# Optimization experiments

Hardware: AMD Instinct MI355X
Metric: run time of the kernel (lower is better)

## Reference

```python
import jax, jax.numpy as jnp
import numpy as np

B, T, C, H = 4, 2048, 1024, 16
D = C // H


def setup_inputs() -> dict:
    key = jax.random.key(0)
    ks = jax.random.split(key, 5)
    s = C ** -0.5  # keep linear outputs O(1) like standard init
    x = jax.random.normal(ks[0], (B, T, C), dtype=jnp.float32)
    Wq = jax.random.normal(ks[1], (C, C), dtype=jnp.float32) * s
    Wk = jax.random.normal(ks[2], (C, C), dtype=jnp.float32) * s
    Wv = jax.random.normal(ks[3], (C, C), dtype=jnp.float32) * s
    Wproj = jax.random.normal(ks[4], (C, C), dtype=jnp.float32) * s
    alpha_raw = jnp.zeros((1, H, 1, 1), dtype=jnp.float32)
    beta_raw = jnp.zeros((1, H, 1, 1), dtype=jnp.float32)
    state = jnp.zeros((B, H, D, D), dtype=jnp.float32)
    return dict(x=x, Wq=Wq, Wk=Wk, Wv=Wv, Wproj=Wproj,
                alpha_raw=alpha_raw, beta_raw=beta_raw, state=state)


def reference(x, Wq, Wk, Wv, Wproj, alpha_raw, beta_raw, state):
    Bx, Tx, Cx = x.shape
    Hn = alpha_raw.shape[1]
    Dh = Cx // Hn
    # projections (torch Linear: x @ W^T), split heads -> (B, H, T, D)
    def proj(W):
        return (x @ W.T).reshape(Bx, Tx, Hn, Dh).transpose(0, 2, 1, 3)
    q, k, v = proj(Wq), proj(Wk), proj(Wv)
    # F.normalize(k, dim=-1) with eps=1e-12
    k = k / jnp.maximum(jnp.linalg.norm(k, axis=-1, keepdims=True), 1e-12)
    alpha = jax.nn.sigmoid(alpha_raw) * 0.5  # (1, H, 1, 1)
    beta = jax.nn.sigmoid(beta_raw) * 0.5

    def step(st, qkv):
        qt, kt, vt = qkv  # each (B, H, D)
        # y_t = q_t @ state^T
        y = jnp.einsum('bhe,bhde->bhd', qt, st)
        # Mk = state @ k_t
        Mk = jnp.einsum('bhde,bhe->bhd', st, kt)
        st = st - alpha * jnp.einsum('bhd,bhe->bhde', Mk, kt) \
                + beta * jnp.einsum('bhd,bhe->bhde', vt, kt)
        return st, y

    # scan over time: (T, B, H, D)
    qT = q.transpose(2, 0, 1, 3)
    kT = k.transpose(2, 0, 1, 3)
    vT = v.transpose(2, 0, 1, 3)
    state_f, ys = jax.lax.scan(step, state, (qT, kT, vT))
    y = ys.transpose(1, 0, 2, 3).reshape(Bx, Tx, Cx)  # (B, T, C)
    out = y @ Wproj.T
    return out, state_f
```

## Files before the change

kernel.cpp:

```cpp
#include <hip/hip_runtime.h>
#include <hip/hip_bf16.h>
#include <cstdint>

#define B_ 4
#define T_ 2048
#define C_ 1024
#define H_ 16
#define D_ 64
#define NC_ 32
#define L_ 64

typedef __attribute__((ext_vector_type(8))) short bf16x8;
typedef __attribute__((ext_vector_type(4))) float f32x4;

static __device__ __forceinline__ unsigned short f2bf(float f) {
  unsigned u = __float_as_uint(f);
  u += 0x7fff + ((u >> 16) & 1);
  return (unsigned short)(u >> 16);
}
static __device__ __forceinline__ float bf2f(unsigned short b) {
  return __uint_as_float(((unsigned)b) << 16);
}
static __device__ __forceinline__ int swz128(int row, int byte) {
  return row * 128 + (byte ^ ((row & 7) << 4));
}

#define LDS_BARRIER() asm volatile("s_waitcnt lgkmcnt(0)\ns_barrier" ::: "memory")

__global__ __launch_bounds__(256) void cvt_kernel(const float* __restrict__ src,
                                                  unsigned short* __restrict__ dst, int n) {
  int i = (blockIdx.x * 256 + threadIdx.x) * 4;
  if (i >= n) return;
  float4 v = *reinterpret_cast<const float4*>(src + i);
  ushort4 o;
  o.x = f2bf(v.x); o.y = f2bf(v.y); o.z = f2bf(v.z); o.w = f2bf(v.w);
  *reinterpret_cast<ushort4*>(dst + i) = o;
}

__global__ __launch_bounds__(256) void cvt_w_kernel(const float* __restrict__ wq,
                                                    const float* __restrict__ wk,
                                                    const float* __restrict__ wv,
                                                    const float* __restrict__ wp,
                                                    unsigned short* __restrict__ W3,
                                                    unsigned short* __restrict__ Wp) {
  const int g = blockIdx.x >> 10;
  const float* src = (g == 0) ? wq : (g == 1) ? wk : (g == 2) ? wv : wp;
  unsigned short* dst = (g < 3) ? (W3 + (long)g * 1048576) : Wp;
  int i = ((blockIdx.x & 1023) * 256 + threadIdx.x) * 4;
  float4 v = *reinterpret_cast<const float4*>(src + i);
  ushort4 o;
  o.x = f2bf(v.x); o.y = f2bf(v.y); o.z = f2bf(v.z); o.w = f2bf(v.w);
  *reinterpret_cast<ushort4*>(dst + i) = o;
}


#define STAGE256(GP, GR0, KT, LOFF) do {                                          \
    const unsigned short* _s = (GP) + ((GR0) + wid * 8 + lr8) * 1024L             \
                               + (long)(KT) * 64 + skb * 8;                       \
    char* _d = (char*)lds + (LOFF) + wid * 1024;                                  \
    __builtin_amdgcn_global_load_lds((const __attribute__((address_space(1))) void*)_s,      \
        (__attribute__((address_space(3))) void*)_d, 16, 0, 0);                   \
    __builtin_amdgcn_global_load_lds((const __attribute__((address_space(1))) void*)(_s + 64 * 1024L), \
        (__attribute__((address_space(3))) void*)(_d + 8192), 16, 0, 0);          \
  } while (0)

#define PHASE256(AO, BO, MH, NH, STG) do {                                        \
    asm volatile("s_waitcnt vmcnt(6)" ::: "memory");                              \
    bf16x8 av[4][2], bv[2][2];                                                    \
    {                                                                             \
      const char* ab = (const char*)lds + (AO) + (MH) * 16384 + arow;             \
      const char* bb = (const char*)lds + (BO) + (NH) * 16384 + brow;             \
      _Pragma("unroll")                                                           \
      for (int j = 0; j < 4; ++j) {                                               \
        av[j][0] = *(const bf16x8*)(ab + j * 4096 + cb0);                         \
        av[j][1] = *(const bf16x8*)(ab + j * 4096 + cb1);                         \
      }                                                                           \
      _Pragma("unroll")                                                           \
      for (int j2 = 0; j2 < 2; ++j2) {                                            \
        bv[j2][0] = *(const bf16x8*)(bb + j2 * 8192 + cb0);                       \
        bv[j2][1] = *(const bf16x8*)(bb + j2 * 8192 + cb1);                       \
      }                                                                           \
    }                                                                             \
    STG;                                                                          \
    __builtin_amdgcn_s_barrier();                                                 \
    asm volatile("s_waitcnt lgkmcnt(0)" ::: "memory");                            \
    __builtin_amdgcn_sched_barrier(0);                                            \
    __builtin_amdgcn_s_setprio(1);                                                \
    _Pragma("unroll")                                                             \
    for (int j = 0; j < 4; ++j)                                                   \
      _Pragma("unroll")                                                           \
      for (int j2 = 0; j2 < 2; ++j2)                                              \
        acc[(MH) * 4 + j][(NH) * 2 + j2] = __builtin_amdgcn_mfma_f32_16x16x32_bf16( \
            av[j][0], bv[j2][0], acc[(MH) * 4 + j][(NH) * 2 + j2], 0, 0, 0);      \
    _Pragma("unroll")                                                             \
    for (int j = 0; j < 4; ++j)                                                   \
      _Pragma("unroll")                                                           \
      for (int j2 = 0; j2 < 2; ++j2)                                              \
        acc[(MH) * 4 + j][(NH) * 2 + j2] = __builtin_amdgcn_mfma_f32_16x16x32_bf16( \
            av[j][1], bv[j2][1], acc[(MH) * 4 + j][(NH) * 2 + j2], 0, 0, 0);      \
    __builtin_amdgcn_s_setprio(0);                                                \
    __builtin_amdgcn_s_barrier();                                                 \
  } while (0)

__global__ __launch_bounds__(512, 2) void gemm256_bt(
    const unsigned short* __restrict__ A,
    const unsigned short* __restrict__ Bw,
    unsigned short* __restrict__ C, int N) {
  __shared__ __align__(16) char lds[131072];
  enum { EA = 0, EB = 32768, OA = 65536, OB = 98304, HF = 16384 };
  const int tid = threadIdx.x;
  const int wid = tid >> 6, lane = tid & 63;
  const int wm = wid >> 2, wn = wid & 3;
  const int f = lane & 15, g = lane >> 4;
  const int lr8 = lane >> 3, lc = lane & 7;
  const int skb = lc ^ lr8;
  const long bM = (long)blockIdx.y * 256;
  const long bN = (long)blockIdx.x * 256;
  const int cb0 = ((0 + g) ^ (f & 7)) * 16;
  const int cb1 = ((4 + g) ^ (f & 7)) * 16;
  const int arow = (wm * 16 + f) * 128;
  const int brow = (wn * 16 + f) * 128;

  f32x4 acc[8][4] = {};

  STAGE256(A, bM, 0, EA);
  STAGE256(Bw, bN, 0, EB);
  STAGE256(A, bM + 128, 0, EA + HF);
  STAGE256(Bw, bN + 128, 0, EB + HF);
  STAGE256(Bw, bN, 1, OB);
  STAGE256(A, bM, 1, OA);
  asm volatile("s_waitcnt vmcnt(8)" ::: "memory");
  __builtin_amdgcn_s_barrier();

  for (int i = 0; i < 8; ++i) {
    const int todd = 2 * i + 1;
    int te = 2 * i + 2; if (te > 14) te = 14;
    int to = 2 * i + 3; if (to > 15) to = 15;
    PHASE256(EA, EB, 0, 0, STAGE256(A, bM + 128, todd, OA + HF));
    PHASE256(EA, EB, 1, 0, STAGE256(Bw, bN + 128, todd, OB + HF));
    PHASE256(EA, EB, 0, 1, STAGE256(Bw, bN, te, EB));
    PHASE256(EA, EB, 1, 1, STAGE256(A, bM, te, EA));
    PHASE256(OA, OB, 0, 0, STAGE256(A, bM + 128, te, EA + HF));
    PHASE256(OA, OB, 1, 0, STAGE256(Bw, bN + 128, te, EB + HF));
    PHASE256(OA, OB, 0, 1, STAGE256(Bw, bN, to, OB));
    PHASE256(OA, OB, 1, 1, STAGE256(A, bM, to, OA));
  }

#pragma unroll
  for (int mf = 0; mf < 8; ++mf) {
    long row = bM + (mf >> 2) * 128 + (mf & 3) * 32 + wm * 16 + g * 4;
#pragma unroll
    for (int nf = 0; nf < 4; ++nf) {
      long col = bN + (nf >> 1) * 128 + (nf & 1) * 64 + wn * 16 + f;
#pragma unroll
      for (int r = 0; r < 4; ++r)
        C[(row + r) * (long)N + col] = f2bf(acc[mf][nf][r]);
    }
  }
}

template<int OUT_BF16>
__global__ __launch_bounds__(256) void gemm_bt(const unsigned short* __restrict__ A,
                                               const unsigned short* __restrict__ Bw,
                                               void* __restrict__ Cp,
                                               int M, int N, int K) {
  __shared__ __align__(16) unsigned short sA[128 * 32];
  __shared__ __align__(16) unsigned short sB[128 * 32];
  const int tid = threadIdx.x;
  const int wid = tid >> 6, lane = tid & 63;
  const int wm = wid >> 1, wn = wid & 1;
  const long blockM = (long)blockIdx.y * 128;
  const long blockN = (long)blockIdx.x * 128;

  f32x4 acc[4][4] = {};

  const int ar = lane >> 2;
  const int ac = (lane & 3) * 8;
  const unsigned short* Abase = A + (blockM + wid * 32 + ar) * (long)K + ac;
  const unsigned short* Bbase = Bw + (blockN + wid * 32 + ar) * (long)K + ac;
  char* sAb = (char*)sA + wid * 2048;
  char* sBb = (char*)sB + wid * 2048;

  for (int k0 = 0; k0 < K; k0 += 32) {
    __syncthreads();
    __builtin_amdgcn_global_load_lds((const __attribute__((address_space(1))) void*)(Abase + k0),
                                     (__attribute__((address_space(3))) void*)(sAb), 16, 0, 0);
    __builtin_amdgcn_global_load_lds((const __attribute__((address_space(1))) void*)(Abase + 16 * (long)K + k0),
                                     (__attribute__((address_space(3))) void*)(sAb + 1024), 16, 0, 0);
    __builtin_amdgcn_global_load_lds((const __attribute__((address_space(1))) void*)(Bbase + k0),
                                     (__attribute__((address_space(3))) void*)(sBb), 16, 0, 0);
    __builtin_amdgcn_global_load_lds((const __attribute__((address_space(1))) void*)(Bbase + 16 * (long)K + k0),
                                     (__attribute__((address_space(3))) void*)(sBb + 1024), 16, 0, 0);
    __syncthreads();

    const int koff = (lane >> 4) * 8;
    const int rA = wm * 64 + (lane & 15);
    const int rB = wn * 64 + (lane & 15);
    bf16x8 af[4], bfr[4];
#pragma unroll
    for (int m = 0; m < 4; ++m)
      af[m] = *reinterpret_cast<const bf16x8*>(&sA[(rA + m * 16) * 32 + koff]);
#pragma unroll
    for (int n = 0; n < 4; ++n)
      bfr[n] = *reinterpret_cast<const bf16x8*>(&sB[(rB + n * 16) * 32 + koff]);
#pragma unroll
    for (int m = 0; m < 4; ++m)
#pragma unroll
      for (int n = 0; n < 4; ++n)
        acc[m][n] = __builtin_amdgcn_mfma_f32_16x16x32_bf16(af[m], bfr[n], acc[m][n], 0, 0, 0);
  }

  const int cr = (lane >> 4) * 4;
  const int cc = lane & 15;
#pragma unroll
  for (int m = 0; m < 4; ++m) {
    long R = blockM + wm * 64 + m * 16 + cr;
#pragma unroll
    for (int n = 0; n < 4; ++n) {
      long Cc = blockN + wn * 64 + n * 16 + cc;
#pragma unroll
      for (int r = 0; r < 4; ++r) {
        if (OUT_BF16)
          ((unsigned short*)Cp)[(R + r) * (long)N + Cc] = f2bf(acc[m][n][r]);
        else
          ((float*)Cp)[(R + r) * (long)N + Cc] = acc[m][n][r];
      }
    }
  }
}

__global__ __launch_bounds__(256) void chunk_prep(
    unsigned short* __restrict__ qkv,
    const float* __restrict__ a_raw, const float* __restrict__ b_raw,
    unsigned short* __restrict__ Ubuf, unsigned short* __restrict__ Wbuf,
    unsigned short* __restrict__ SLbuf) {
  __shared__ __align__(16) unsigned short sK[64 * 64];
  __shared__ __align__(16) unsigned short sQ[64 * 64];
  __shared__ __align__(16) unsigned short sV[64 * 64];
  __shared__ float sA[64 * 64];

  const int blk = blockIdx.x;
  const int bh = blk >> 5, c = blk & 31;
  const int b = bh >> 4, h = bh & 15;
  const int tid = threadIdx.x;
  const int wid = tid >> 6, lane = tid & 63;

  const float alpha = 0.5f / (1.f + __expf(-a_raw[h]));
  const float beta  = 0.5f / (1.f + __expf(-b_raw[h]));

  {
    const int row = tid >> 2, cg = tid & 3;
    unsigned short* gp = qkv + (long)(b * 2048 + c * 64 + row) * 3072 + h * 64 + cg * 16;
    bf16x8 q0 = *(const bf16x8*)(gp);
    bf16x8 q1 = *(const bf16x8*)(gp + 8);
    bf16x8 k0 = *(const bf16x8*)(gp + 1024);
    bf16x8 k1 = *(const bf16x8*)(gp + 1024 + 8);
    bf16x8 v0 = *(const bf16x8*)(gp + 2048);
    bf16x8 v1 = *(const bf16x8*)(gp + 2048 + 8);
    float kf[16];
    float ss = 0.f;
#pragma unroll
    for (int i = 0; i < 8; ++i) { kf[i] = bf2f((unsigned short)k0[i]); ss += kf[i] * kf[i]; }
#pragma unroll
    for (int i = 0; i < 8; ++i) { kf[8 + i] = bf2f((unsigned short)k1[i]); ss += kf[8 + i] * kf[8 + i]; }
    ss += __shfl_xor(ss, 1);
    ss += __shfl_xor(ss, 2);
    const float inv = 1.f / fmaxf(sqrtf(ss), 1e-12f);
    bf16x8 n0, n1;
#pragma unroll
    for (int i = 0; i < 8; ++i) { n0[i] = (short)f2bf(kf[i] * inv); n1[i] = (short)f2bf(kf[8 + i] * inv); }
    *(bf16x8*)((char*)sK + swz128(row, cg * 32)) = n0;
    *(bf16x8*)((char*)sK + swz128(row, cg * 32 + 16)) = n1;
    *(bf16x8*)(gp + 1024) = n0;
    *(bf16x8*)(gp + 1024 + 8) = n1;
    *(bf16x8*)((char*)sQ + swz128(row, cg * 32)) = q0;
    *(bf16x8*)((char*)sQ + swz128(row, cg * 32 + 16)) = q1;
    *(bf16x8*)((char*)sV + row * 128 + cg * 32) = v0;
    *(bf16x8*)((char*)sV + row * 128 + cg * 32 + 16) = v1;
  }
  __syncthreads();

  const int rfrag = lane & 15, koff = (lane >> 4) * 8, crow = (lane >> 4) * 4;
  const int w2 = wid & 1;
  if (wid < 2) {
#pragma unroll
    for (int mt = 0; mt < 2; ++mt) {
      const int m = w2 * 2 + mt;
      const int ra = 16 * m + rfrag;
      f32x4 acc[4] = {};
#pragma unroll
      for (int ks = 0; ks < 2; ++ks) {
        bf16x8 af = *(const bf16x8*)((const char*)sK + swz128(ra, ks * 64 + koff * 2));
#pragma unroll
        for (int n = 0; n < 4; ++n) {
          bf16x8 bf = *(const bf16x8*)((const char*)sK + swz128(16 * n + rfrag, ks * 64 + koff * 2));
          acc[n] = __builtin_amdgcn_mfma_f32_16x16x32_bf16(af, bf, acc[n], 0, 0, 0);
        }
      }
#pragma unroll
      for (int n = 0; n < 4; ++n)
#pragma unroll
        for (int r = 0; r < 4; ++r)
          sA[(16 * m + crow + r) * 64 + 16 * n + rfrag] = acc[n][r];
    }
  } else {
#pragma unroll
    for (int mt = 0; mt < 2; ++mt) {
      const int m = w2 * 2 + mt;
      const int ra = 16 * m + rfrag;
      f32x4 acc[4] = {};
#pragma unroll
      for (int ks = 0; ks < 2; ++ks) {
        bf16x8 af = *(const bf16x8*)((const char*)sQ + swz128(ra, ks * 64 + koff * 2));
#pragma unroll
        for (int n = 0; n < 4; ++n) {
          bf16x8 bf = *(const bf16x8*)((const char*)sK + swz128(16 * n + rfrag, ks * 64 + koff * 2));
          acc[n] = __builtin_amdgcn_mfma_f32_16x16x32_bf16(af, bf, acc[n], 0, 0, 0);
        }
      }
#pragma unroll
      for (int n = 0; n < 4; ++n)
#pragma unroll
        for (int r = 0; r < 4; ++r) {
          int t = 16 * m + crow + r, j = 16 * n + rfrag;
          SLbuf[(long)blk * 4096 + t * 64 + j] = (j < t) ? f2bf(acc[n][r]) : (unsigned short)0;
        }
    }
  }
  __syncthreads();

  if (wid < 2) {
    const int d = lane;
    float x[64];
#pragma unroll
    for (int t = 0; t < 64; ++t) {
      float rhs;
      if (wid == 0) rhs = beta * bf2f(sV[t * 64 + d]);
      else          rhs = alpha * bf2f(*(const unsigned short*)((const char*)sK + swz128(t, 2 * d)));
      float s = 0.f;
#pragma unroll
      for (int j = 0; j < t; ++j) s = fmaf(sA[t * 64 + j], x[j], s);
      x[t] = rhs - alpha * s;
    }
    unsigned short* ob = (wid == 0 ? Ubuf : Wbuf) + (long)blk * 4096 + d;
#pragma unroll
    for (int t = 0; t < 64; ++t) ob[t * 64] = f2bf(x[t]);
  }
}

__global__ __launch_bounds__(256) void chunk_scan(
    const unsigned short* __restrict__ qkv,
    const unsigned short* __restrict__ Ubuf, const unsigned short* __restrict__ Wbuf,
    const unsigned short* __restrict__ SLbuf,
    const float* __restrict__ state_in, unsigned short* __restrict__ ybuf,
    float* __restrict__ state_out) {
  __shared__ __align__(16) unsigned short sQ[64 * 64];
  __shared__ __align__(16) unsigned short sW[64 * 64];
  __shared__ __align__(16) unsigned short sSL[64 * 64];
  __shared__ __align__(16) unsigned short sKT[64 * 64];
  __shared__ __align__(16) unsigned short sU[64 * 16];
  __shared__ __align__(16) unsigned short sGT[16 * 64];
  __shared__ __align__(16) unsigned short sS[16 * 64];

  const int blk = blockIdx.x;
  const int bh = blk >> 2, dq = blk & 3;
  const int b = bh >> 4, h = bh & 15;
  const int tid = threadIdx.x, wid = tid >> 6, lane = tid & 63;
  const int rfrag = lane & 15, koff = (lane >> 4) * 8, crow = (lane >> 4) * 4;
  const int row = tid >> 2, cg = tid & 3;

  const unsigned short* gpb = qkv + (long)(b * 2048 + row) * 3072 + h * 64 + cg * 16;
  const long tbb = ((long)(bh * 32) * 64 + row) * 64 + cg * 16;
  const long ubb = ((long)(bh * 32) * 64 + (tid >> 1)) * 64 + dq * 16 + (tid & 1) * 8;

  bf16x8 qv0, qv1, kv0, kv1, wv0, wv1, sl0, sl1, uv;
  {
    qv0 = *(const bf16x8*)gpb;
    qv1 = *(const bf16x8*)(gpb + 8);
    kv0 = *(const bf16x8*)(gpb + 1024);
    kv1 = *(const bf16x8*)(gpb + 1024 + 8);
    wv0 = *(const bf16x8*)(Wbuf + tbb);
    wv1 = *(const bf16x8*)(Wbuf + tbb + 8);
    sl0 = *(const bf16x8*)(SLbuf + tbb);
    sl1 = *(const bf16x8*)(SLbuf + tbb + 8);
    uv = (tid < 128) ? *(const bf16x8*)(Ubuf + ubb) : bf16x8{};
  }

  f32x4 sacc;
#pragma unroll
  for (int r = 0; r < 4; ++r)
    sacc[r] = state_in[(long)bh * 4096 + (dq * 16 + crow + r) * 64 + 16 * wid + rfrag];
#pragma unroll
  for (int r = 0; r < 4; ++r)
    *(unsigned short*)((char*)sS + swz128(crow + r, 2 * (16 * wid + rfrag))) = f2bf(sacc[r]);

  for (int c = 0; c < NC_; ++c) {
    *(bf16x8*)((char*)sQ + swz128(row, cg * 32)) = qv0;
    *(bf16x8*)((char*)sQ + swz128(row, cg * 32 + 16)) = qv1;
    *(bf16x8*)((char*)sW + swz128(row, cg * 32)) = wv0;
    *(bf16x8*)((char*)sW + swz128(row, cg * 32 + 16)) = wv1;
    *(bf16x8*)((char*)sSL + swz128(row, cg * 32)) = sl0;
    *(bf16x8*)((char*)sSL + swz128(row, cg * 32 + 16)) = sl1;
#pragma unroll
    for (int i = 0; i < 8; ++i) {
      *(unsigned short*)((char*)sKT + swz128(cg * 16 + i, 2 * row)) = (unsigned short)kv0[i];
      *(unsigned short*)((char*)sKT + swz128(cg * 16 + 8 + i, 2 * row)) = (unsigned short)kv1[i];
    }
    if (tid < 128) *(bf16x8*)((char*)sU + ((tid >> 1) * 16 + (tid & 1) * 8) * 2) = uv;

    {
      const int cn = (c + 1 < NC_) ? c + 1 : c;
      const unsigned short* gp = gpb + (long)cn * 64 * 3072;
      const long tb = tbb + (long)cn * 4096;
      qv0 = *(const bf16x8*)gp;
      qv1 = *(const bf16x8*)(gp + 8);
      kv0 = *(const bf16x8*)(gp + 1024);
      kv1 = *(const bf16x8*)(gp + 1024 + 8);
      wv0 = *(const bf16x8*)(Wbuf + tb);
      wv1 = *(const bf16x8*)(Wbuf + tb + 8);
      sl0 = *(const bf16x8*)(SLbuf + tb);
      sl1 = *(const bf16x8*)(SLbuf + tb + 8);
      if (tid < 128) uv = *(const bf16x8*)(Ubuf + ubb + (long)cn * 4096);
    }
    LDS_BARRIER();

    const int ta = 16 * wid + rfrag;
    f32x4 p = {};
    f32x4 yac = {};
#pragma unroll
    for (int ks = 0; ks < 2; ++ks) {
      bf16x8 afw = *(const bf16x8*)((const char*)sW + swz128(ta, ks * 64 + koff * 2));
      bf16x8 afq = *(const bf16x8*)((const char*)sQ + swz128(ta, ks * 64 + koff * 2));
      bf16x8 bS = *(const bf16x8*)((const char*)sS + swz128(rfrag, ks * 64 + koff * 2));
      p = __builtin_amdgcn_mfma_f32_16x16x32_bf16(afw, bS, p, 0, 0, 0);
      yac = __builtin_amdgcn_mfma_f32_16x16x32_bf16(afq, bS, yac, 0, 0, 0);
    }
#pragma unroll
    for (int r = 0; r < 4; ++r) {
      int t = 16 * wid + crow + r;
      float gg = bf2f(sU[t * 16 + rfrag]) - p[r];
      *(unsigned short*)((char*)sGT + swz128(rfrag, 2 * t)) = f2bf(gg);
    }
    LDS_BARRIER();

#pragma unroll
    for (int ks = 0; ks < 2; ++ks) {
      bf16x8 aSL = *(const bf16x8*)((const char*)sSL + swz128(ta, ks * 64 + koff * 2));
      bf16x8 bGT = *(const bf16x8*)((const char*)sGT + swz128(rfrag, ks * 64 + koff * 2));
      yac = __builtin_amdgcn_mfma_f32_16x16x32_bf16(aSL, bGT, yac, 0, 0, 0);
    }
#pragma unroll
    for (int r = 0; r < 4; ++r) {
      int t = 16 * wid + crow + r;
      ybuf[(long)(b * 2048 + c * 64 + t) * 1024 + h * 64 + dq * 16 + rfrag] = f2bf(yac[r]);
    }
#pragma unroll
    for (int ks = 0; ks < 2; ++ks) {
      bf16x8 aGT = *(const bf16x8*)((const char*)sGT + swz128(rfrag, ks * 64 + koff * 2));
      bf16x8 bKT = *(const bf16x8*)((const char*)sKT + swz128(16 * wid + rfrag, ks * 64 + koff * 2));
      sacc = __builtin_amdgcn_mfma_f32_16x16x32_bf16(aGT, bKT, sacc, 0, 0, 0);
    }
    LDS_BARRIER();

#pragma unroll
    for (int r = 0; r < 4; ++r)
      *(unsigned short*)((char*)sS + swz128(crow + r, 2 * (16 * wid + rfrag))) = f2bf(sacc[r]);
  }

#pragma unroll
  for (int r = 0; r < 4; ++r)
    state_out[(long)bh * 4096 + (dq * 16 + crow + r) * 64 + 16 * wid + rfrag] = sacc[r];
}

extern "C" void kernel_launch(void* const* d_in, const int* in_sizes, int n_in,
                              void* d_out, int out_size, void* d_ws, size_t ws_size,
                              hipStream_t stream) {
  (void)in_sizes; (void)n_in; (void)out_size; (void)ws_size;
  const float* x     = (const float*)d_in[0];
  const float* Wq    = (const float*)d_in[1];
  const float* Wk    = (const float*)d_in[2];
  const float* Wv    = (const float*)d_in[3];
  const float* Wproj = (const float*)d_in[4];
  const float* a_raw = (const float*)d_in[5];
  const float* b_raw = (const float*)d_in[6];
  const float* state = (const float*)d_in[7];

  char* ws = (char*)d_ws;
  unsigned short* xbf = (unsigned short*)ws;
  unsigned short* W3  = (unsigned short*)(ws + (16l << 20));
  unsigned short* Wp  = (unsigned short*)(ws + (22l << 20));
  unsigned short* qkv = (unsigned short*)(ws + (24l << 20));
  unsigned short* Ub  = (unsigned short*)(ws + (72l << 20));
  unsigned short* Wb  = (unsigned short*)(ws + (88l << 20));
  unsigned short* SLb = (unsigned short*)(ws + (104l << 20));
  float* out = (float*)d_out;
  float* state_out = out + (long)B_ * T_ * C_;

  cvt_kernel<<<dim3(8192), dim3(256), 0, stream>>>(x, xbf, 8388608);
  cvt_w_kernel<<<dim3(4096), dim3(256), 0, stream>>>(Wq, Wk, Wv, Wproj, W3, Wp);

  gemm256_bt<<<dim3(3072 / 256, 8192 / 256), dim3(512), 0, stream>>>(xbf, W3, qkv, 3072);

  chunk_prep<<<dim3(2048), dim3(256), 0, stream>>>(qkv, a_raw, b_raw, Ub, Wb, SLb);
  chunk_scan<<<dim3(256), dim3(256), 0, stream>>>(qkv, Ub, Wb, SLb, state, xbf, state_out);

  gemm_bt<0><<<dim3(1024 / 128, 8192 / 128), dim3(256), 0, stream>>>(xbf, Wp, (void*)out, 8192, 1024, 1024);
}
```

Before: 209.5 us.

## Restructure chunk scan to one block per head with double-buffered LDS tiles

The chunk_scan kernel now uses one 256-thread block per (batch, head) instead of four blocks that split the state rows. Each wave owns a 16-row slice of the state and computes the full 64-token chunk against its own private slice, so the intra-chunk barrier between the G computation and its use goes away. Chunk tiles are double-buffered in a 96KB LDS array and global loads are prefetched two chunks ahead, leaving one barrier per chunk. The cost is a grid of only 64 blocks on a GPU with many more CUs, plus four times the MFMA work per wave, so parallelism drops in exchange for fewer barriers and better latency hiding.

```diff
diff --git a/kernel.cpp b/kernel.cpp
--- a/kernel.cpp
+++ b/kernel.cpp
@@ -52,7 +52,6 @@
   o.x = f2bf(v.x); o.y = f2bf(v.y); o.z = f2bf(v.z); o.w = f2bf(v.w);
   *reinterpret_cast<ushort4*>(dst + i) = o;
 }
-
 
 #define STAGE256(GP, GR0, KT, LOFF) do {                                          \
     const unsigned short* _s = (GP) + ((GR0) + wid * 8 + lr8) * 1024L             \
@@ -354,122 +353,142 @@
     const unsigned short* __restrict__ SLbuf,
     const float* __restrict__ state_in, unsigned short* __restrict__ ybuf,
     float* __restrict__ state_out) {
-  __shared__ __align__(16) unsigned short sQ[64 * 64];
-  __shared__ __align__(16) unsigned short sW[64 * 64];
-  __shared__ __align__(16) unsigned short sSL[64 * 64];
-  __shared__ __align__(16) unsigned short sKT[64 * 64];
-  __shared__ __align__(16) unsigned short sU[64 * 16];
-  __shared__ __align__(16) unsigned short sGT[16 * 64];
-  __shared__ __align__(16) unsigned short sS[16 * 64];
-
-  const int blk = blockIdx.x;
-  const int bh = blk >> 2, dq = blk & 3;
+  __shared__ __align__(16) char lds[98304];
+  const int bh = blockIdx.x;
   const int b = bh >> 4, h = bh & 15;
   const int tid = threadIdx.x, wid = tid >> 6, lane = tid & 63;
-  const int rfrag = lane & 15, koff = (lane >> 4) * 8, crow = (lane >> 4) * 4;
+  const int f = lane & 15, koff = (lane >> 4) * 8, crow = (lane >> 4) * 4;
   const int row = tid >> 2, cg = tid & 3;
+  const int dq = wid;
+
+  char* gt = lds + 81920 + wid * 2048;
+  char* ss = lds + 90112 + wid * 2048;
 
   const unsigned short* gpb = qkv + (long)(b * 2048 + row) * 3072 + h * 64 + cg * 16;
   const long tbb = ((long)(bh * 32) * 64 + row) * 64 + cg * 16;
-  const long ubb = ((long)(bh * 32) * 64 + (tid >> 1)) * 64 + dq * 16 + (tid & 1) * 8;
-
-  bf16x8 qv0, qv1, kv0, kv1, wv0, wv1, sl0, sl1, uv;
-  {
-    qv0 = *(const bf16x8*)gpb;
-    qv1 = *(const bf16x8*)(gpb + 8);
-    kv0 = *(const bf16x8*)(gpb + 1024);
-    kv1 = *(const bf16x8*)(gpb + 1024 + 8);
-    wv0 = *(const bf16x8*)(Wbuf + tbb);
-    wv1 = *(const bf16x8*)(Wbuf + tbb + 8);
-    sl0 = *(const bf16x8*)(SLbuf + tbb);
-    sl1 = *(const bf16x8*)(SLbuf + tbb + 8);
-    uv = (tid < 128) ? *(const bf16x8*)(Ubuf + ubb) : bf16x8{};
-  }
-
-  f32x4 sacc;
-#pragma unroll
-  for (int r = 0; r < 4; ++r)
-    sacc[r] = state_in[(long)bh * 4096 + (dq * 16 + crow + r) * 64 + 16 * wid + rfrag];
-#pragma unroll
-  for (int r = 0; r < 4; ++r)
-    *(unsigned short*)((char*)sS + swz128(crow + r, 2 * (16 * wid + rfrag))) = f2bf(sacc[r]);
+
+  bf16x8 qv0, qv1, kv0, kv1, wv0, wv1, sl0, sl1, uv0, uv1;
+#define LOADREGS(CN) do {                                                     \
+    const unsigned short* gp = gpb + (long)(CN) * 64 * 3072;                  \
+    const long tb = tbb + (long)(CN) * 4096;                                  \
+    qv0 = *(const bf16x8*)gp;            qv1 = *(const bf16x8*)(gp + 8);      \
+    kv0 = *(const bf16x8*)(gp + 1024);   kv1 = *(const bf16x8*)(gp + 1032);   \
+    wv0 = *(const bf16x8*)(Wbuf + tb);   wv1 = *(const bf16x8*)(Wbuf + tb + 8); \
+    sl0 = *(const bf16x8*)(SLbuf + tb);  sl1 = *(const bf16x8*)(SLbuf + tb + 8); \
+    uv0 = *(const bf16x8*)(Ubuf + tb);   uv1 = *(const bf16x8*)(Ubuf + tb + 8); \
+  } while (0)
+
+#define WRITE_TILES(BUF) do {                                                 \
+    char* bp = lds + (BUF) * 40960;                                           \
+    *(bf16x8*)(bp + swz128(row, cg * 32)) = qv0;                              \
+    *(bf16x8*)(bp + swz128(row, cg * 32 + 16)) = qv1;                         \
+    *(bf16x8*)(bp + 8192 + swz128(row, cg * 32)) = wv0;                       \
+    *(bf16x8*)(bp + 8192 + swz128(row, cg * 32 + 16)) = wv1;                  \
+    *(bf16x8*)(bp + 16384 + swz128(row, cg * 32)) = sl0;                      \
+    *(bf16x8*)(bp + 16384 + swz128(row, cg * 32 + 16)) = sl1;                 \
+    _Pragma("unroll")                                                         \
+    for (int i = 0; i < 8; ++i) {                                             \
+      *(unsigned short*)(bp + 24576 + swz128(cg * 16 + i, 2 * row)) = (unsigned short)kv0[i]; \
+      *(unsigned short*)(bp + 24576 + swz128(cg * 16 + 8 + i, 2 * row)) = (unsigned short)kv1[i]; \
+    }                                                                         \
+    *(bf16x8*)(bp + 32768 + swz128(row, cg * 32)) = uv0;                      \
+    *(bf16x8*)(bp + 32768 + swz128(row, cg * 32 + 16)) = uv1;                 \
+  } while (0)
+
+  f32x4 sacc[4];
+#pragma unroll
+  for (int nn = 0; nn < 4; ++nn)
+#pragma unroll
+    for (int r = 0; r < 4; ++r)
+      sacc[nn][r] = state_in[(long)bh * 4096 + (dq * 16 + crow + r) * 64 + nn * 16 + f];
+#pragma unroll
+  for (int nn = 0; nn < 4; ++nn)
+#pragma unroll
+    for (int r = 0; r < 4; ++r)
+      *(unsigned short*)(ss + swz128(crow + r, 2 * (nn * 16 + f))) = f2bf(sacc[nn][r]);
+
+  LOADREGS(0);
+  WRITE_TILES(0);
+  LOADREGS(1);
+  LDS_BARRIER();
 
   for (int c = 0; c < NC_; ++c) {
-    *(bf16x8*)((char*)sQ + swz128(row, cg * 32)) = qv0;
-    *(bf16x8*)((char*)sQ + swz128(row, cg * 32 + 16)) = qv1;
-    *(bf16x8*)((char*)sW + swz128(row, cg * 32)) = wv0;
-    *(bf16x8*)((char*)sW + swz128(row, cg * 32 + 16)) = wv1;
-    *(bf16x8*)((char*)sSL + swz128(row, cg * 32)) = sl0;
-    *(bf16x8*)((char*)sSL + swz128(row, cg * 32 + 16)) = sl1;
-#pragma unroll
-    for (int i = 0; i < 8; ++i) {
-      *(unsigned short*)((char*)sKT + swz128(cg * 16 + i, 2 * row)) = (unsigned short)kv0[i];
-      *(unsigned short*)((char*)sKT + swz128(cg * 16 + 8 + i, 2 * row)) = (unsigned short)kv1[i];
-    }
-    if (tid < 128) *(bf16x8*)((char*)sU + ((tid >> 1) * 16 + (tid & 1) * 8) * 2) = uv;
-
+    const int cur = c & 1;
+    if (c + 1 < NC_) WRITE_TILES(cur ^ 1);
     {
-      const int cn = (c + 1 < NC_) ? c + 1 : c;
-      const unsigned short* gp = gpb + (long)cn * 64 * 3072;
-      const long tb = tbb + (long)cn * 4096;
-      qv0 = *(const bf16x8*)gp;
-      qv1 = *(const bf16x8*)(gp + 8);
-      kv0 = *(const bf16x8*)(gp + 1024);
-      kv1 = *(const bf16x8*)(gp + 1024 + 8);
-      wv0 = *(const bf16x8*)(Wbuf + tb);
-      wv1 = *(const bf16x8*)(Wbuf + tb + 8);
-      sl0 = *(const bf16x8*)(SLbuf + tb);
-      sl1 = *(const bf16x8*)(SLbuf + tb + 8);
-      if (tid < 128) uv = *(const bf16x8*)(Ubuf + ubb + (long)cn * 4096);
-    }
+      int cn = c + 2; if (cn > NC_ - 1) cn = NC_ - 1;
+      LOADREGS(cn);
+    }
+
+    const char* bp = lds + cur * 40960;
+    bf16x8 bs0 = *(const bf16x8*)(ss + swz128(f, koff * 2));
+    bf16x8 bs1 = *(const bf16x8*)(ss + swz128(f, 64 + koff * 2));
+
+    f32x4 p[4];
+#pragma unroll
+    for (int m = 0; m < 4; ++m) {
+      bf16x8 a0 = *(const bf16x8*)(bp + 8192 + swz128(m * 16 + f, koff * 2));
+      bf16x8 a1 = *(const bf16x8*)(bp + 8192 + swz128(m * 16 + f, 64 + koff * 2));
+      f32x4 z = {};
+      z = __builtin_amdgcn_mfma_f32_16x16x32_bf16(a0, bs0, z, 0, 0, 0);
+      p[m] = __builtin_amdgcn_mfma_f32_16x16x32_bf16(a1, bs1, z, 0, 0, 0);
+    }
+#pragma unroll
+    for (int m = 0; m < 4; ++m)
+#pragma unroll
+      for (int r = 0; r < 4; ++r) {
+        int t = m * 16 + crow + r;
+        float u = bf2f(*(const unsigned short*)(bp + 32768 + swz128(t, 2 * (dq * 16 + f))));
+        *(unsigned short*)(gt + swz128(f, 2 * t)) = f2bf(u - p[m][r]);
+      }
+    f32x4 yac[4];
+#pragma unroll
+    for (int m = 0; m < 4; ++m) {
+      bf16x8 a0 = *(const bf16x8*)(bp + swz128(m * 16 + f, koff * 2));
+      bf16x8 a1 = *(const bf16x8*)(bp + swz128(m * 16 + f, 64 + koff * 2));
+      f32x4 z = {};
+      z = __builtin_amdgcn_mfma_f32_16x16x32_bf16(a0, bs0, z, 0, 0, 0);
+      yac[m] = __builtin_amdgcn_mfma_f32_16x16x32_bf16(a1, bs1, z, 0, 0, 0);
+    }
+    bf16x8 g0 = *(const bf16x8*)(gt + swz128(f, koff * 2));
+    bf16x8 g1 = *(const bf16x8*)(gt + swz128(f, 64 + koff * 2));
+#pragma unroll
+    for (int m = 0; m < 4; ++m) {
+      bf16x8 a0 = *(const bf16x8*)(bp + 16384 + swz128(m * 16 + f, koff * 2));
+      bf16x8 a1 = *(const bf16x8*)(bp + 16384 + swz128(m * 16 + f, 64 + koff * 2));
+      yac[m] = __builtin_amdgcn_mfma_f32_16x16x32_bf16(a0, g0, yac[m], 0, 0, 0);
+      yac[m] = __builtin_amdgcn_mfma_f32_16x16x32_bf16(a1, g1, yac[m], 0, 0, 0);
+    }
+#pragma unroll
+    for (int nn = 0; nn < 4; ++nn) {
+      bf16x8 b0 = *(const bf16x8*)(bp + 24576 + swz128(nn * 16 + f, koff * 2));
+      bf16x8 b1 = *(const bf16x8*)(bp + 24576 + swz128(nn * 16 + f, 64 + koff * 2));
+      sacc[nn] = __builtin_amdgcn_mfma_f32_16x16x32_bf16(g0, b0, sacc[nn], 0, 0, 0);
+      sacc[nn] = __builtin_amdgcn_mfma_f32_16x16x32_bf16(g1, b1, sacc[nn], 0, 0, 0);
+    }
+#pragma unroll
+    for (int m = 0; m < 4; ++m)
+#pragma unroll
+      for (int r = 0; r < 4; ++r) {
+        int t = m * 16 + crow + r;
+        ybuf[(long)(b * 2048 + c * 64 + t) * 1024 + h * 64 + dq * 16 + f] = f2bf(yac[m][r]);
+      }
+#pragma unroll
+    for (int nn = 0; nn < 4; ++nn)
+#pragma unroll
+      for (int r = 0; r < 4; ++r)
+        *(unsigned short*)(ss + swz128(crow + r, 2 * (nn * 16 + f))) = f2bf(sacc[nn][r]);
+
     LDS_BARRIER();
-
-    const int ta = 16 * wid + rfrag;
-    f32x4 p = {};
-    f32x4 yac = {};
-#pragma unroll
-    for (int ks = 0; ks < 2; ++ks) {
-      bf16x8 afw = *(const bf16x8*)((const char*)sW + swz128(ta, ks * 64 + koff * 2));
-      bf16x8 afq = *(const bf16x8*)((const char*)sQ + swz128(ta, ks * 64 + koff * 2));
-      bf16x8 bS = *(const bf16x8*)((const char*)sS + swz128(rfrag, ks * 64 + koff * 2));
-      p = __builtin_amdgcn_mfma_f32_16x16x32_bf16(afw, bS, p, 0, 0, 0);
-      yac = __builtin_amdgcn_mfma_f32_16x16x32_bf16(afq, bS, yac, 0, 0, 0);
-    }
-#pragma unroll
-    for (int r = 0; r < 4; ++r) {
-      int t = 16 * wid + crow + r;
-      float gg = bf2f(sU[t * 16 + rfrag]) - p[r];
-      *(unsigned short*)((char*)sGT + swz128(rfrag, 2 * t)) = f2bf(gg);
-    }
-    LDS_BARRIER();
-
-#pragma unroll
-    for (int ks = 0; ks < 2; ++ks) {
-      bf16x8 aSL = *(const bf16x8*)((const char*)sSL + swz128(ta, ks * 64 + koff * 2));
-      bf16x8 bGT = *(const bf16x8*)((const char*)sGT + swz128(rfrag, ks * 64 + koff * 2));
-      yac = __builtin_amdgcn_mfma_f32_16x16x32_bf16(aSL, bGT, yac, 0, 0, 0);
-    }
-#pragma unroll
-    for (int r = 0; r < 4; ++r) {
-      int t = 16 * wid + crow + r;
-      ybuf[(long)(b * 2048 + c * 64 + t) * 1024 + h * 64 + dq * 16 + rfrag] = f2bf(yac[r]);
-    }
-#pragma unroll
-    for (int ks = 0; ks < 2; ++ks) {
-      bf16x8 aGT = *(const bf16x8*)((const char*)sGT + swz128(rfrag, ks * 64 + koff * 2));
-      bf16x8 bKT = *(const bf16x8*)((const char*)sKT + swz128(16 * wid + rfrag, ks * 64 + koff * 2));
-      sacc = __builtin_amdgcn_mfma_f32_16x16x32_bf16(aGT, bKT, sacc, 0, 0, 0);
-    }
-    LDS_BARRIER();
-
+  }
+
+#pragma unroll
+  for (int nn = 0; nn < 4; ++nn)
 #pragma unroll
     for (int r = 0; r < 4; ++r)
-      *(unsigned short*)((char*)sS + swz128(crow + r, 2 * (16 * wid + rfrag))) = f2bf(sacc[r]);
-  }
-
-#pragma unroll
-  for (int r = 0; r < 4; ++r)
-    state_out[(long)bh * 4096 + (dq * 16 + crow + r) * 64 + 16 * wid + rfrag] = sacc[r];
+      state_out[(long)bh * 4096 + (dq * 16 + crow + r) * 64 + nn * 16 + f] = sacc[nn][r];
+#undef LOADREGS
+#undef WRITE_TILES
 }
 
 extern "C" void kernel_launch(void* const* d_in, const int* in_sizes, int n_in,
@@ -502,7 +521,7 @@
   gemm256_bt<<<dim3(3072 / 256, 8192 / 256), dim3(512), 0, stream>>>(xbf, W3, qkv, 3072);
 
   chunk_prep<<<dim3(2048), dim3(256), 0, stream>>>(qkv, a_raw, b_raw, Ub, Wb, SLb);
-  chunk_scan<<<dim3(256), dim3(256), 0, stream>>>(qkv, Ub, Wb, SLb, state, xbf, state_out);
+  chunk_scan<<<dim3(64), dim3(256), 0, stream>>>(qkv, Ub, Wb, SLb, state, xbf, state_out);
 
   gemm_bt<0><<<dim3(1024 / 128, 8192 / 128), dim3(256), 0, stream>>>(xbf, Wp, (void*)out, 8192, 1024, 1024);
 }
```

Result: slower. 223.3 us (+6.6%).
